# Optimization experiments

Hardware: AMD Instinct MI355X
Metric: run time of the kernel (lower is better)

The kernel has to match this reference:

```python
import jax, jax.numpy as jnp
import numpy as np

B, S, E = 8, 2048, 768
N, H = 12, 64
INIT = 0.02
IGNORE = -100000.0


def setup_inputs() -> dict:
    key = jax.random.key(0)
    ks = jax.random.split(key, 5)
    return {
        "normalized_resid_pre": jax.random.normal(ks[0], (B, S, E), jnp.float32),
        "W_Q": jax.random.normal(ks[1], (N, E, H), jnp.float32) * INIT,
        "W_K": jax.random.normal(ks[2], (N, E, H), jnp.float32) * INIT,
        "W_V": jax.random.normal(ks[3], (N, E, H), jnp.float32) * INIT,
        "W_O": jax.random.normal(ks[4], (N, H, E), jnp.float32) * INIT,
        "b_Q": jnp.zeros((N, H), jnp.float32),
        "b_K": jnp.zeros((N, H), jnp.float32),
        "b_V": jnp.zeros((N, H), jnp.float32),
        "b_O": jnp.zeros((E,), jnp.float32),
    }


def reference(normalized_resid_pre, W_Q, W_K, W_V, W_O, b_Q, b_K, b_V, b_O):
    x = normalized_resid_pre
    b, s, e = x.shape
    d_head = W_Q.shape[-1]
    q = jnp.einsum('bse,neh->bsnh', x, W_Q) + b_Q  # [b, sq, n, h]
    k = jnp.einsum('bse,neh->bsnh', x, W_K) + b_K
    v = jnp.einsum('bse,neh->bsnh', x, W_V) + b_V
    scores = jnp.einsum('bqnh,bknh->bnqk', q, k) / jnp.sqrt(jnp.float32(d_head))
    mask = jnp.tril(jnp.ones((s, s), jnp.float32))  # [sq, sk]
    masked = mask * scores + (1.0 - mask) * IGNORE
    probs = jax.nn.softmax(masked, axis=-1)
    z = jnp.einsum('bnqk,bknh->bqnh', probs, v)
    # sum over heads of per-head output projection + bias
    out = jnp.einsum('bqnh,nhe->bqe', z, W_O) + b_O
    return out
```

## Files before the change

### kernel.cpp

```cpp
#include <hip/hip_runtime.h>
#include <hip/hip_bf16.h>
#include <stdint.h>


#define B_ 8
#define S_ 2048
#define E_ 768
#define NHEADS 12
#define HD 64
#define BS (B_*S_)
#define NHD (NHEADS*HD)

typedef short bf16x8 __attribute__((ext_vector_type(8)));
typedef short bf16x4 __attribute__((ext_vector_type(4)));
typedef float f32x4  __attribute__((ext_vector_type(4)));
typedef __hip_bfloat16 bf16;

__device__ __forceinline__ f32x4 mfma16(bf16x8 a, bf16x8 b, f32x4 c) {
    return __builtin_amdgcn_mfma_f32_16x16x32_bf16(a, b, c, 0, 0, 0);
}
__device__ __forceinline__ bf16x8 ld8(const bf16* p) {
    return *reinterpret_cast<const bf16x8*>(p);
}
__device__ __forceinline__ bf16x8 pack8(f32x4 a, f32x4 b) {
    union { bf16x8 v; __hip_bfloat162 h[4]; } u;
    u.h[0] = __float22bfloat162_rn(make_float2(a[0], a[1]));
    u.h[1] = __float22bfloat162_rn(make_float2(a[2], a[3]));
    u.h[2] = __float22bfloat162_rn(make_float2(b[0], b[1]));
    u.h[3] = __float22bfloat162_rn(make_float2(b[2], b[3]));
    return u.v;
}


__global__ __launch_bounds__(256) void prep_kernel(
    const float* __restrict__ x,  const float* __restrict__ Wq,
    const float* __restrict__ Wk, const float* __restrict__ Wv,
    const float* __restrict__ Wo,
    bf16* __restrict__ xp,  bf16* __restrict__ WTp, bf16* __restrict__ WoTp)
{
    const int tid = blockIdx.x * 256 + threadIdx.x;
    const int nth = gridDim.x * 256;

    for (int c = tid; c < BS*E_/8; c += nth) {
        const int r  = c / 96;
        const int k8 = (c - r*96) * 8;
        const float4 f0 = *reinterpret_cast<const float4*>(x + (size_t)r*E_ + k8);
        const float4 f1 = *reinterpret_cast<const float4*>(x + (size_t)r*E_ + k8 + 4);
        union { bf16x8 v; __hip_bfloat162 h[4]; } u;
        u.h[0] = __float22bfloat162_rn(make_float2(f0.x, f0.y));
        u.h[1] = __float22bfloat162_rn(make_float2(f0.z, f0.w));
        u.h[2] = __float22bfloat162_rn(make_float2(f1.x, f1.y));
        u.h[3] = __float22bfloat162_rn(make_float2(f1.z, f1.w));
        const size_t dst = (size_t)((r>>4)*24 + (k8>>5))*512
                         + (size_t)((((k8>>3)&3)<<4) + (r&15))*8;
        *reinterpret_cast<bf16x8*>(xp + dst) = u.v;
    }

    for (int c2 = tid; c2 < NHD*96; c2 += nth) {
        const int r  = c2 / 96;
        const int e8 = (c2 - r*96) * 8;
        const int n = r >> 6, h = r & 63;
        const float* sq = Wq + (size_t)(n*E_ + e8)*HD + h;
        const float* sk = Wk + (size_t)(n*E_ + e8)*HD + h;
        const float* sv = Wv + (size_t)(n*E_ + e8)*HD + h;
        union { bf16x8 v; bf16 el[8]; } uq, uk, uv;
        #pragma unroll
        for (int j = 0; j < 8; ++j) {
            uq.el[j] = __float2bfloat16(sq[(size_t)j*HD]);
            uk.el[j] = __float2bfloat16(sk[(size_t)j*HD]);
            uv.el[j] = __float2bfloat16(sv[(size_t)j*HD]);
        }
        const size_t sub = (size_t)(e8>>5)*512
                         + (size_t)((((e8>>3)&3)<<4) + (r&15))*8;
        const size_t rg  = (size_t)(r>>4);
        *reinterpret_cast<bf16x8*>(WTp + ((0*48 + rg)*24)*512 + sub) = uq.v;
        *reinterpret_cast<bf16x8*>(WTp + ((1*48 + rg)*24)*512 + sub) = uk.v;
        *reinterpret_cast<bf16x8*>(WTp + ((2*48 + rg)*24)*512 + sub) = uv.v;
    }

    for (int c3 = tid; c3 < E_*96; c3 += nth) {
        const int e  = c3 / 96;
        const int c8 = (c3 - e*96) * 8;
        union { bf16x8 v; bf16 el[8]; } u;
        #pragma unroll
        for (int j = 0; j < 8; ++j)
            u.el[j] = __float2bfloat16(Wo[(size_t)(c8 + j)*E_ + e]);
        const size_t dst = (size_t)((e>>4)*24 + (c8>>5))*512
                         + (size_t)((((c8>>3)&3)<<4) + (e&15))*8;
        *reinterpret_cast<bf16x8*>(WoTp + dst) = u.v;
    }
}


#define LOAD_A(dst, base, kt, NM)                                                 \
    _Pragma("unroll") for (int m = 0; m < NM; ++m)                                \
    _Pragma("unroll") for (int ks = 0; ks < 2; ++ks)                              \
        dst[m][ks] = ld8((base) + ((size_t)m*24 + (kt)*2 + ks)*512);

#define MFMA_BLK(af, bfv, NM, NN)                                                 \
    _Pragma("unroll") for (int ks = 0; ks < 2; ++ks)                              \
    _Pragma("unroll") for (int m = 0; m < NM; ++m)                                \
    _Pragma("unroll") for (int n = 0; n < NN; ++n)                                \
        acc[m][n] = mfma16(af[m][ks], bfv[n][ks], acc[m][n]);

#define DIRECT_PIPE_BODY(Abase, Bbase, NM, NN)                                    \
    f32x4 acc[NM][NN];                                                            \
    _Pragma("unroll") for (int mf = 0; mf < NM; ++mf)                             \
    _Pragma("unroll") for (int nf = 0; nf < NN; ++nf)                             \
        acc[mf][nf] = (f32x4){0.f, 0.f, 0.f, 0.f};                                \
    bf16x8 a0[NM][2], b0[NN][2], a1[NM][2], b1[NN][2];                            \
    LOAD_A(a0, Abase, 0, NM); LOAD_A(b0, Bbase, 0, NN);                           \
    _Pragma("unroll 1")                                                           \
    for (int kk = 0; kk < 6; ++kk) {                                              \
        const int ktA = 2*kk + 1;                                                 \
        const int ktB = (2*kk + 2 < 12) ? 2*kk + 2 : 11;                          \
        LOAD_A(a1, Abase, ktA, NM); LOAD_A(b1, Bbase, ktA, NN);                   \
        __builtin_amdgcn_sched_barrier(0);                                        \
        MFMA_BLK(a0, b0, NM, NN);                                                 \
        LOAD_A(a0, Abase, ktB, NM); LOAD_A(b0, Bbase, ktB, NN);                   \
        __builtin_amdgcn_sched_barrier(0);                                        \
        MFMA_BLK(a1, b1, NM, NN);                                                 \
    }

__global__ __launch_bounds__(256, 2) void qkv_gemm_p(
    const bf16* __restrict__ xp, const bf16* __restrict__ WTp,
    const float* __restrict__ bq, const float* __restrict__ bk, const float* __restrict__ bv,
    bf16* __restrict__ Qb, bf16* __restrict__ Kb, bf16* __restrict__ VTb)
{
    const int tm = blockIdx.x, tn = blockIdx.y;
    const int lane = threadIdx.x & 63;
    const int w    = threadIdx.x >> 6;
    const int wm = w >> 1, wn = w & 1;
    const int l16 = lane & 15, quad = lane >> 4;
    const bf16* Abase = xp  + ((size_t)(tm*8 + wm*4)*24)*512 + lane*8;
    const bf16* Bbase = WTp + ((size_t)(tn*8 + wn*4)*24)*512 + lane*8;

    DIRECT_PIPE_BODY(Abase, Bbase, 4, 4);

    const int mat = tn / 6;
    const int cloc0 = (tn - mat*6)*128 + wn*64;
    const float* bias = (mat==0) ? bq : (mat==1) ? bk : bv;
    const float scale = (mat==0) ? 0.125f * 1.44269504088896340736f : 1.0f;
    bf16* dstQK = (mat==0) ? Qb : Kb;
    #pragma unroll
    for (int nf = 0; nf < 4; ++nf) {
        const int col = cloc0 + nf*16 + l16;
        const int hn = col >> 6, h = col & 63;
        const float bb = bias[col];
        #pragma unroll
        for (int mf = 0; mf < 4; ++mf) {
            const int row = tm*128 + wm*64 + mf*16 + quad*4;
            const int bi = row >> 11;
            const int s  = row & (S_-1);
            if (mat < 2) {
                bf16* d = dstQK + ((size_t)(bi*NHEADS + hn)*S_ + s)*HD + h;
                #pragma unroll
                for (int r = 0; r < 4; ++r)
                    d[(size_t)r*HD] = __float2bfloat16((acc[mf][nf][r] + bb)*scale);
            } else {
                bf16* d = VTb + ((size_t)(bi*NHEADS + hn)*HD + h)*S_ + s;
                union { bf16x4 v; bf16 e[4]; } u;
                #pragma unroll
                for (int r = 0; r < 4; ++r) u.e[r] = __float2bfloat16(acc[mf][nf][r] + bb);
                *reinterpret_cast<bf16x4*>(d) = u.v;
            }
        }
    }
}

__global__ __launch_bounds__(256, 2) void out_gemm_p(
    const bf16* __restrict__ Zp, const bf16* __restrict__ WoTp,
    const float* __restrict__ bo, float* __restrict__ out)
{
    const int tm = blockIdx.x, tn = blockIdx.y;
    const int lane = threadIdx.x & 63;
    const int w    = threadIdx.x >> 6;
    const int wm = w >> 1, wn = w & 1;
    const int l16 = lane & 15, quad = lane >> 4;
    const bf16* Abase = Zp   + ((size_t)(tm*8 + wm*4)*24)*512 + lane*8;
    const bf16* Bbase = WoTp + ((size_t)(tn*6 + wn*3)*24)*512 + lane*8;

    DIRECT_PIPE_BODY(Abase, Bbase, 4, 3);

    #pragma unroll
    for (int nf = 0; nf < 3; ++nf) {
        const int col = tn*96 + wn*48 + nf*16 + l16;
        const float bb = bo[col];
        #pragma unroll
        for (int mf = 0; mf < 4; ++mf) {
            const int row = tm*128 + wm*64 + mf*16 + quad*4;
            float* d = out + (size_t)row*E_ + col;
            #pragma unroll
            for (int r = 0; r < 4; ++r)
                d[(size_t)r*E_] = acc[mf][nf][r] + bb;
        }
    }
}

__global__ __launch_bounds__(256, 3) void attn_kernel(
    const bf16* __restrict__ Qb, const bf16* __restrict__ Kb,
    const bf16* __restrict__ VTb, bf16* __restrict__ Zp)
{
    __shared__ __align__(16) bf16 sK[2][64*64];
    __shared__ __align__(16) bf16 sV[2][64*64];

    const int id = blockIdx.x;
    const int bx = id / 96;
    const int g  = id - bx*96;
    const int hn = g % NHEADS, b = g / NHEADS;
    const int tid  = threadIdx.x;
    const int w    = tid >> 6;
    const int lane = tid & 63;
    const int l16 = lane & 15, quad = lane >> 4;
    const size_t bn = (size_t)b*NHEADS + hn;

    const bf16* Qbase = Qb  + bn*S_*HD;
    const bf16* Kbase = Kb  + bn*S_*HD;
    const bf16* Vbase = VTb + bn*HD*S_;

    const int mA = tid, mB = tid + 256;
    const int rA = mA >> 3, cgA = mA & 7;
    const int rB = mB >> 3, cgB = mB & 7;
    const int slA = (rA*8 + ((cgA + rA + (rA>>3)) & 7)) * 8;
    const int slB = (rB*8 + ((cgB + rB + (rB>>3)) & 7)) * 8;
    const size_t vofA = (size_t)rA*S_ + cgA*8;
    const size_t vofB = (size_t)rB*S_ + cgB*8;

    const int kperm = (l16 >> 2)*8 + (l16 & 3);
    int kidx[2][2][2];
    #pragma unroll
    for (int c=0;c<2;c++)
        #pragma unroll
        for (int bg=0;bg<2;bg++)
            #pragma unroll
            for (int hf=0;hf<2;hf++) {
                const int r = 32*c + 4*bg + kperm;
                const int q = hf*4 + quad;
                kidx[c][bg][hf] = (r*8 + ((q + r + (r>>3)) & 7)) * 8;
            }
    int vidx[4][2];
    #pragma unroll
    for (int ht=0;ht<4;ht++)
        #pragma unroll
        for (int c=0;c<2;c++) {
            const int rho = ht*16 + l16;
            const int q = c*4 + quad;
            vidx[ht][c] = (rho*8 + ((q + rho + (rho>>3)) & 7)) * 8;
        }

    #pragma unroll
    for (int half = 0; half < 2; ++half) {
        const int qblk = half ? (S_/128 - 1 - bx) : bx;
        const int ktb  = 2*qblk + 1;
        const int ktw  = 2*qblk + (w >> 1);
        const int qbase = qblk*128 + w*32;

        bf16x8 bqf[2][2];
        #pragma unroll
        for (int qi=0;qi<2;qi++)
            #pragma unroll
            for (int hf=0;hf<2;hf++)
                bqf[qi][hf] = ld8(Qbase + (size_t)(qbase + qi*16 + l16)*HD + hf*32 + quad*8);

        f32x4 acc[2][4];
        #pragma unroll
        for (int qi=0;qi<2;qi++)
            #pragma unroll
            for (int ht=0;ht<4;ht++) acc[qi][ht] = (f32x4){0.f,0.f,0.f,0.f};
        float lsum[2] = {0.f, 0.f};

        bf16x8 k0 = ld8(Kbase + (size_t)mA*8);
        bf16x8 k1 = ld8(Kbase + (size_t)mB*8);
        bf16x8 v0 = ld8(Vbase + vofA);
        bf16x8 v1 = ld8(Vbase + vofB);
        *reinterpret_cast<bf16x8*>(&sK[0][slA]) = k0;
        *reinterpret_cast<bf16x8*>(&sK[0][slB]) = k1;
        *reinterpret_cast<bf16x8*>(&sV[0][slA]) = v0;
        *reinterpret_cast<bf16x8*>(&sV[0][slB]) = v1;
        __syncthreads();

        for (int kt = 0; kt <= ktb; ++kt) {
            if (kt < ktb) {
                const size_t kt1 = (size_t)(kt+1)*64;
                k0 = ld8(Kbase + kt1*HD + (size_t)mA*8);
                k1 = ld8(Kbase + kt1*HD + (size_t)mB*8);
                v0 = ld8(Vbase + vofA + kt1);
                v1 = ld8(Vbase + vofB + kt1);
            }
            if (kt <= ktw) {
                const bf16* kb = sK[kt & 1];
                const bf16* vb = sV[kt & 1];
                #pragma unroll
                for (int c=0;c<2;c++) {
                    const bf16x8 akA0 = ld8(kb + kidx[c][0][0]);
                    const bf16x8 akA1 = ld8(kb + kidx[c][0][1]);
                    const bf16x8 akB0 = ld8(kb + kidx[c][1][0]);
                    const bf16x8 akB1 = ld8(kb + kidx[c][1][1]);
                    bf16x8 av[4];
                    #pragma unroll
                    for (int ht=0;ht<4;ht++) av[ht] = ld8(vb + vidx[ht][c]);

                    #pragma unroll
                    for (int qi=0;qi<2;qi++) {
                        f32x4 s0 = (f32x4){0.f,0.f,0.f,0.f};
                        s0 = mfma16(akA0, bqf[qi][0], s0);
                        s0 = mfma16(akA1, bqf[qi][1], s0);
                        f32x4 s1 = (f32x4){0.f,0.f,0.f,0.f};
                        s1 = mfma16(akB0, bqf[qi][0], s1);
                        s1 = mfma16(akB1, bqf[qi][1], s1);
                        if (kt == ktw) {
                            const int q  = qbase + qi*16 + l16;
                            const int kb0 = kt*64 + c*32 + quad*8;
                            #pragma unroll
                            for (int r=0;r<4;r++) {
                                s0[r] = (kb0 + r     > q) ? -1e30f : s0[r];
                                s1[r] = (kb0 + 4 + r > q) ? -1e30f : s1[r];
                            }
                        }
                        float ls = 0.f;
                        #pragma unroll
                        for (int r=0;r<4;r++) {
                            s0[r] = __builtin_amdgcn_exp2f(s0[r]);
                            s1[r] = __builtin_amdgcn_exp2f(s1[r]);
                            ls += s0[r] + s1[r];
                        }
                        lsum[qi] += ls;
                        const bf16x8 pf = pack8(s0, s1);
                        #pragma unroll
                        for (int ht=0;ht<4;ht++)
                            acc[qi][ht] = mfma16(av[ht], pf, acc[qi][ht]);
                    }
                }
            }
            if (kt < ktb) {
                const int nb = (kt+1) & 1;
                *reinterpret_cast<bf16x8*>(&sK[nb][slA]) = k0;
                *reinterpret_cast<bf16x8*>(&sK[nb][slB]) = k1;
                *reinterpret_cast<bf16x8*>(&sV[nb][slA]) = v0;
                *reinterpret_cast<bf16x8*>(&sV[nb][slB]) = v1;
            }
            __syncthreads();
        }

        #pragma unroll
        for (int qi=0;qi<2;qi++) {
            float rs = lsum[qi];
            rs += __shfl_xor(rs, 16, 64);
            rs += __shfl_xor(rs, 32, 64);
            const float inv_l = 1.0f / rs;
            const int rowg = b*128 + (qbase >> 4) + qi;
            #pragma unroll
            for (int ht=0;ht<4;ht++) {
                union { bf16x4 v; bf16 e[4]; } u;
                #pragma unroll
                for (int r=0;r<4;r++) u.e[r] = __float2bfloat16(acc[qi][ht][r] * inv_l);
                const int k = hn*64 + ht*16 + quad*4;
                bf16* d = Zp + ((size_t)rowg*24 + (k>>5))*512
                             + (size_t)((((k>>3)&3)<<4) + l16)*8 + (k&7);
                *reinterpret_cast<bf16x4*>(d) = u.v;
            }
        }
    }
}

extern "C" void kernel_launch(void* const* d_in, const int* in_sizes, int n_in,
                              void* d_out, int out_size, void* d_ws, size_t ws_size,
                              hipStream_t stream)
{
    const float* x  = (const float*)d_in[0];
    const float* Wq = (const float*)d_in[1];
    const float* Wk = (const float*)d_in[2];
    const float* Wv = (const float*)d_in[3];
    const float* Wo = (const float*)d_in[4];
    const float* bq = (const float*)d_in[5];
    const float* bk = (const float*)d_in[6];
    const float* bv = (const float*)d_in[7];
    const float* bo = (const float*)d_in[8];
    float* out = (float*)d_out;

    char* ws = (char*)d_ws;
    size_t off = 0;
    auto alloc = [&](size_t bytes){ char* p = ws + off; off += (bytes + 255) & ~(size_t)255; return p; };
    bf16* xp   = (bf16*)alloc((size_t)BS*E_*2);
    bf16* WTp  = (bf16*)alloc((size_t)3*NHD*E_*2);
    bf16* WoTp = (bf16*)alloc((size_t)E_*NHD*2);
    bf16* Qb   = (bf16*)alloc((size_t)BS*NHD*2);
    bf16* Kb   = (bf16*)alloc((size_t)BS*NHD*2);
    bf16* VTb  = (bf16*)alloc((size_t)BS*NHD*2);
    bf16* Zp   = (bf16*)alloc((size_t)BS*NHD*2);

    prep_kernel<<<4096, 256, 0, stream>>>(x, Wq, Wk, Wv, Wo, xp, WTp, WoTp);
    qkv_gemm_p<<<dim3(BS/128, 18), 256, 0, stream>>>(xp, WTp, bq, bk, bv, Qb, Kb, VTb);
    attn_kernel<<<768, 256, 0, stream>>>(Qb, Kb, VTb, Zp);
    out_gemm_p<<<dim3(BS/128, 8), 256, 0, stream>>>(Zp, WoTp, bo, out);
}
```

Baseline: 234.2 us.

## Triple-buffer K/V shared tiles with two-ahead prefetch and MFMA priority hints

Moves the attention kernel's K/V staging from a double buffer to a three-slot rotating LDS ring. Global loads are issued two tiles ahead, and the LDS store of the next tile happens at the top of each iteration rather than after compute. It also raises wave priority around the MFMA groups with s_setprio so matrix work from one wave is favoured over other waves' memory or ALU work. The goal is to hide more global-load latency. In exchange LDS use grows from 32KB to 48KB per block, which may reduce occupancy under launch_bounds(256,3). The initial prefetch of tile 1 also reads past the end of the tile range when ktb is 0.

```diff
diff --git a/kernel.cpp b/kernel.cpp
--- a/kernel.cpp
+++ b/kernel.cpp
@@ -201,8 +201,8 @@
     const bf16* __restrict__ Qb, const bf16* __restrict__ Kb,
     const bf16* __restrict__ VTb, bf16* __restrict__ Zp)
 {
-    __shared__ __align__(16) bf16 sK[2][64*64];
-    __shared__ __align__(16) bf16 sV[2][64*64];
+    __shared__ __align__(16) bf16 sK[3*4096];
+    __shared__ __align__(16) bf16 sV[3*4096];
 
     const int id = blockIdx.x;
     const int bx = id / 96;
@@ -273,23 +273,36 @@
         bf16x8 k1 = ld8(Kbase + (size_t)mB*8);
         bf16x8 v0 = ld8(Vbase + vofA);
         bf16x8 v1 = ld8(Vbase + vofB);
-        *reinterpret_cast<bf16x8*>(&sK[0][slA]) = k0;
-        *reinterpret_cast<bf16x8*>(&sK[0][slB]) = k1;
-        *reinterpret_cast<bf16x8*>(&sV[0][slA]) = v0;
-        *reinterpret_cast<bf16x8*>(&sV[0][slB]) = v1;
+        *reinterpret_cast<bf16x8*>(&sK[slA]) = k0;
+        *reinterpret_cast<bf16x8*>(&sK[slB]) = k1;
+        *reinterpret_cast<bf16x8*>(&sV[slA]) = v0;
+        *reinterpret_cast<bf16x8*>(&sV[slB]) = v1;
+        k0 = ld8(Kbase + 4096 + (size_t)mA*8);
+        k1 = ld8(Kbase + 4096 + (size_t)mB*8);
+        v0 = ld8(Vbase + vofA + 64);
+        v1 = ld8(Vbase + vofB + 64);
         __syncthreads();
 
+        int rd = 0, wr = 1, l3 = 2;
         for (int kt = 0; kt <= ktb; ++kt) {
-            if (kt < ktb) {
-                const size_t kt1 = (size_t)(kt+1)*64;
-                k0 = ld8(Kbase + kt1*HD + (size_t)mA*8);
-                k1 = ld8(Kbase + kt1*HD + (size_t)mB*8);
-                v0 = ld8(Vbase + vofA + kt1);
-                v1 = ld8(Vbase + vofB + kt1);
+            if (kt + 1 <= ktb) {
+                bf16* kw = sK + wr*4096;
+                bf16* vw = sV + wr*4096;
+                *reinterpret_cast<bf16x8*>(&kw[slA]) = k0;
+                *reinterpret_cast<bf16x8*>(&kw[slB]) = k1;
+                *reinterpret_cast<bf16x8*>(&vw[slA]) = v0;
+                *reinterpret_cast<bf16x8*>(&vw[slB]) = v1;
+            }
+            if (kt + 2 <= ktb) {
+                const size_t o = (size_t)(kt + 2) * 64;
+                k0 = ld8(Kbase + o*HD + (size_t)mA*8);
+                k1 = ld8(Kbase + o*HD + (size_t)mB*8);
+                v0 = ld8(Vbase + vofA + o);
+                v1 = ld8(Vbase + vofB + o);
             }
             if (kt <= ktw) {
-                const bf16* kb = sK[kt & 1];
-                const bf16* vb = sV[kt & 1];
+                const bf16* kb = sK + rd*4096;
+                const bf16* vb = sV + rd*4096;
                 #pragma unroll
                 for (int c=0;c<2;c++) {
                     const bf16x8 akA0 = ld8(kb + kidx[c][0][0]);
@@ -302,12 +315,14 @@
 
                     #pragma unroll
                     for (int qi=0;qi<2;qi++) {
+                        __builtin_amdgcn_s_setprio(1);
                         f32x4 s0 = (f32x4){0.f,0.f,0.f,0.f};
                         s0 = mfma16(akA0, bqf[qi][0], s0);
                         s0 = mfma16(akA1, bqf[qi][1], s0);
                         f32x4 s1 = (f32x4){0.f,0.f,0.f,0.f};
                         s1 = mfma16(akB0, bqf[qi][0], s1);
                         s1 = mfma16(akB1, bqf[qi][1], s1);
+                        __builtin_amdgcn_s_setprio(0);
                         if (kt == ktw) {
                             const int q  = qbase + qi*16 + l16;
                             const int kb0 = kt*64 + c*32 + quad*8;
@@ -326,20 +341,16 @@
                         }
                         lsum[qi] += ls;
                         const bf16x8 pf = pack8(s0, s1);
+                        __builtin_amdgcn_s_setprio(1);
                         #pragma unroll
                         for (int ht=0;ht<4;ht++)
                             acc[qi][ht] = mfma16(av[ht], pf, acc[qi][ht]);
+                        __builtin_amdgcn_s_setprio(0);
                     }
                 }
             }
-            if (kt < ktb) {
-                const int nb = (kt+1) & 1;
-                *reinterpret_cast<bf16x8*>(&sK[nb][slA]) = k0;
-                *reinterpret_cast<bf16x8*>(&sK[nb][slB]) = k1;
-                *reinterpret_cast<bf16x8*>(&sV[nb][slA]) = v0;
-                *reinterpret_cast<bf16x8*>(&sV[nb][slB]) = v1;
-            }
             __syncthreads();
+            const int t = rd; rd = wr; wr = l3; l3 = t;
         }
 
         #pragma unroll
```

After: 232.8 us. Within noise of the previous version (-0.6%).

## Pre-swizzle K/V into MFMA fragment layout and drop LDS staging in attention

Applied to the files above, without the earlier changes.

The QKV GEMM epilogue now writes K and V directly in a packed per-fragment layout, so each lane can load MFMA operands from global memory with one 16-byte load. The attention kernel drops the shared-memory double buffer and __syncthreads, and each wave now handles 64 query rows independently with a register-level software pipeline over 32-key chunks. This removes LDS traffic and block-wide barriers, at the cost of more register pressure (occupancy hint lowered to 2) and scattered 2-byte stores for K in the GEMM epilogue. Each wave now reads K/V from global or L2 on its own instead of sharing one staged copy per block.

```diff
diff --git a/kernel.cpp b/kernel.cpp
--- a/kernel.cpp
+++ b/kernel.cpp
@@ -125,7 +125,7 @@
 __global__ __launch_bounds__(256, 2) void qkv_gemm_p(
     const bf16* __restrict__ xp, const bf16* __restrict__ WTp,
     const float* __restrict__ bq, const float* __restrict__ bk, const float* __restrict__ bv,
-    bf16* __restrict__ Qb, bf16* __restrict__ Kb, bf16* __restrict__ VTb)
+    bf16* __restrict__ Qb, bf16* __restrict__ Kp, bf16* __restrict__ Vp)
 {
     const int tm = blockIdx.x, tn = blockIdx.y;
     const int lane = threadIdx.x & 63;
@@ -141,7 +141,6 @@
     const int cloc0 = (tn - mat*6)*128 + wn*64;
     const float* bias = (mat==0) ? bq : (mat==1) ? bk : bv;
     const float scale = (mat==0) ? 0.125f * 1.44269504088896340736f : 1.0f;
-    bf16* dstQK = (mat==0) ? Qb : Kb;
     #pragma unroll
     for (int nf = 0; nf < 4; ++nf) {
         const int col = cloc0 + nf*16 + l16;
@@ -152,16 +151,33 @@
             const int row = tm*128 + wm*64 + mf*16 + quad*4;
             const int bi = row >> 11;
             const int s  = row & (S_-1);
-            if (mat < 2) {
-                bf16* d = dstQK + ((size_t)(bi*NHEADS + hn)*S_ + s)*HD + h;
+            const size_t headbase = (size_t)(bi*NHEADS + hn)*256*512;
+            if (mat == 0) {
+                bf16* d = Qb + ((size_t)(bi*NHEADS + hn)*S_ + s)*HD + h;
                 #pragma unroll
                 for (int r = 0; r < 4; ++r)
                     d[(size_t)r*HD] = __float2bfloat16((acc[mf][nf][r] + bb)*scale);
+            } else if (mat == 1) {
+                const int hf = h >> 5, kq = (h >> 3) & 3, e = h & 7;
+                #pragma unroll
+                for (int r = 0; r < 4; ++r) {
+                    const int sr = s + r;
+                    const int gg = sr >> 5, kv5 = sr & 31;
+                    const int bg = (kv5 >> 2) & 1;
+                    const int rl = ((kv5 >> 3) << 2) | (kv5 & 3);
+                    Kp[headbase + (size_t)(gg*4 + bg*2 + hf)*512 + (kq*16 + rl)*8 + e]
+                        = __float2bfloat16(acc[mf][nf][r] + bb);
+                }
             } else {
-                bf16* d = VTb + ((size_t)(bi*NHEADS + hn)*HD + h)*S_ + s;
+                const int dg = (h >> 4) & 3;
+                const int rl = h & 15;
+                const int gg = s >> 5;
+                const int kq = (s >> 3) & 3;
+                const int e0 = s & 7;
                 union { bf16x4 v; bf16 e[4]; } u;
                 #pragma unroll
                 for (int r = 0; r < 4; ++r) u.e[r] = __float2bfloat16(acc[mf][nf][r] + bb);
+                bf16* d = Vp + headbase + (size_t)(gg*4 + dg)*512 + (kq*16 + rl)*8 + e0;
                 *reinterpret_cast<bf16x4*>(d) = u.v;
             }
         }
@@ -197,170 +213,113 @@
     }
 }
 
-__global__ __launch_bounds__(256, 3) void attn_kernel(
-    const bf16* __restrict__ Qb, const bf16* __restrict__ Kb,
-    const bf16* __restrict__ VTb, bf16* __restrict__ Zp)
-{
-    __shared__ __align__(16) bf16 sK[2][64*64];
-    __shared__ __align__(16) bf16 sV[2][64*64];
-
+__global__ __launch_bounds__(256, 2) void attn_kernel(
+    const bf16* __restrict__ Qb, const bf16* __restrict__ Kp,
+    const bf16* __restrict__ Vp, bf16* __restrict__ Zp)
+{
     const int id = blockIdx.x;
     const int bx = id / 96;
-    const int g  = id - bx*96;
-    const int hn = g % NHEADS, b = g / NHEADS;
-    const int tid  = threadIdx.x;
-    const int w    = tid >> 6;
-    const int lane = tid & 63;
+    const int hc = id - bx*96;
+    const int hn = hc % NHEADS, b = hc / NHEADS;
+    const int w    = threadIdx.x >> 6;
+    const int lane = threadIdx.x & 63;
     const int l16 = lane & 15, quad = lane >> 4;
     const size_t bn = (size_t)b*NHEADS + hn;
 
-    const bf16* Qbase = Qb  + bn*S_*HD;
-    const bf16* Kbase = Kb  + bn*S_*HD;
-    const bf16* Vbase = VTb + bn*HD*S_;
-
-    const int mA = tid, mB = tid + 256;
-    const int rA = mA >> 3, cgA = mA & 7;
-    const int rB = mB >> 3, cgB = mB & 7;
-    const int slA = (rA*8 + ((cgA + rA + (rA>>3)) & 7)) * 8;
-    const int slB = (rB*8 + ((cgB + rB + (rB>>3)) & 7)) * 8;
-    const size_t vofA = (size_t)rA*S_ + cgA*8;
-    const size_t vofB = (size_t)rB*S_ + cgB*8;
-
-    const int kperm = (l16 >> 2)*8 + (l16 & 3);
-    int kidx[2][2][2];
-    #pragma unroll
-    for (int c=0;c<2;c++)
-        #pragma unroll
-        for (int bg=0;bg<2;bg++)
+    const int qblk = (w >> 1) ? (15 - bx) : bx;
+    const int wsub = w & 1;
+    const int qbase = qblk*128 + wsub*64;
+    const int jmax  = 2*(2*qblk + wsub) + 1;
+
+    const bf16* Qbase = Qb + bn*(size_t)S_*HD;
+    const bf16* Kh = Kp + bn*(size_t)256*512;
+    const bf16* Vh = Vp + bn*(size_t)256*512;
+
+    bf16x8 bqf[4][2];
+    #pragma unroll
+    for (int qi = 0; qi < 4; ++qi)
+        #pragma unroll
+        for (int hf = 0; hf < 2; ++hf)
+            bqf[qi][hf] = ld8(Qbase + (size_t)(qbase + qi*16 + l16)*HD + hf*32 + quad*8);
+
+    f32x4 acc[4][4];
+    #pragma unroll
+    for (int qi = 0; qi < 4; ++qi)
+        #pragma unroll
+        for (int ht = 0; ht < 4; ++ht) acc[qi][ht] = (f32x4){0.f,0.f,0.f,0.f};
+    float lsum[4] = {0.f, 0.f, 0.f, 0.f};
+
+#define LD_KV(ks, vs, gj) do {                                                    \
+    _Pragma("unroll") for (int f = 0; f < 4; ++f)                                 \
+        ks[f] = ld8(Kh + ((size_t)(gj)*4 + f)*512 + lane*8);                      \
+    _Pragma("unroll") for (int f = 0; f < 4; ++f)                                 \
+        vs[f] = ld8(Vh + ((size_t)(gj)*4 + f)*512 + lane*8);                      \
+} while (0)
+
+#define ATT_COMPUTE(ks, vs, j) do {                                               \
+    const int kvbase = (j) * 32;                                                  \
+    const bool diag = (kvbase + 31 > qbase);                                      \
+    _Pragma("unroll")                                                             \
+    for (int qi = 0; qi < 4; ++qi) {                                              \
+        f32x4 s0 = (f32x4){0.f,0.f,0.f,0.f};                                      \
+        s0 = mfma16(ks[0], bqf[qi][0], s0);                                       \
+        s0 = mfma16(ks[1], bqf[qi][1], s0);                                       \
+        f32x4 s1 = (f32x4){0.f,0.f,0.f,0.f};                                      \
+        s1 = mfma16(ks[2], bqf[qi][0], s1);                                       \
+        s1 = mfma16(ks[3], bqf[qi][1], s1);                                       \
+        if (diag) {                                                               \
+            const int q   = qbase + qi*16 + l16;                                  \
+            const int kb0 = kvbase + quad*8;                                      \
+            _Pragma("unroll") for (int r = 0; r < 4; ++r) {                       \
+                s0[r] = (kb0 + r     > q) ? -1e30f : s0[r];                       \
+                s1[r] = (kb0 + 4 + r > q) ? -1e30f : s1[r];                       \
+            }                                                                     \
+        }                                                                         \
+        float ls = 0.f;                                                           \
+        _Pragma("unroll") for (int r = 0; r < 4; ++r) {                           \
+            s0[r] = __builtin_amdgcn_exp2f(s0[r]);                                \
+            s1[r] = __builtin_amdgcn_exp2f(s1[r]);                                \
+            ls += s0[r] + s1[r];                                                  \
+        }                                                                         \
+        lsum[qi] += ls;                                                           \
+        const bf16x8 pf = pack8(s0, s1);                                          \
+        _Pragma("unroll") for (int ht = 0; ht < 4; ++ht)                          \
+            acc[qi][ht] = mfma16(vs[ht], pf, acc[qi][ht]);                        \
+    }                                                                             \
+} while (0)
+
+    bf16x8 k0[4], v0[4], k1[4], v1[4];
+    LD_KV(k0, v0, 0);
+    #pragma unroll 1
+    for (int j = 0; j < jmax; j += 2) {
+        LD_KV(k1, v1, j + 1);
+        __builtin_amdgcn_sched_barrier(0);
+        ATT_COMPUTE(k0, v0, j);
+        if (j + 2 <= jmax) { LD_KV(k0, v0, j + 2); }
+        __builtin_amdgcn_sched_barrier(0);
+        ATT_COMPUTE(k1, v1, j + 1);
+    }
+
+    #pragma unroll
+    for (int qi = 0; qi < 4; ++qi) {
+        float rs = lsum[qi];
+        rs += __shfl_xor(rs, 16, 64);
+        rs += __shfl_xor(rs, 32, 64);
+        const float inv_l = 1.0f / rs;
+        const int rowg = b*128 + (qbase >> 4) + qi;
+        #pragma unroll
+        for (int ht = 0; ht < 4; ++ht) {
+            union { bf16x4 v; bf16 e[4]; } u;
             #pragma unroll
-            for (int hf=0;hf<2;hf++) {
-                const int r = 32*c + 4*bg + kperm;
-                const int q = hf*4 + quad;
-                kidx[c][bg][hf] = (r*8 + ((q + r + (r>>3)) & 7)) * 8;
-            }
-    int vidx[4][2];
-    #pragma unroll
-    for (int ht=0;ht<4;ht++)
-        #pragma unroll
-        for (int c=0;c<2;c++) {
-            const int rho = ht*16 + l16;
-            const int q = c*4 + quad;
-            vidx[ht][c] = (rho*8 + ((q + rho + (rho>>3)) & 7)) * 8;
+            for (int r = 0; r < 4; ++r) u.e[r] = __float2bfloat16(acc[qi][ht][r] * inv_l);
+            const int k = hn*64 + ht*16 + quad*4;
+            bf16* d = Zp + ((size_t)rowg*24 + (k>>5))*512
+                         + (size_t)((((k>>3)&3)<<4) + l16)*8 + (k&7);
+            *reinterpret_cast<bf16x4*>(d) = u.v;
         }
-
-    #pragma unroll
-    for (int half = 0; half < 2; ++half) {
-        const int qblk = half ? (S_/128 - 1 - bx) : bx;
-        const int ktb  = 2*qblk + 1;
-        const int ktw  = 2*qblk + (w >> 1);
-        const int qbase = qblk*128 + w*32;
-
-        bf16x8 bqf[2][2];
-        #pragma unroll
-        for (int qi=0;qi<2;qi++)
-            #pragma unroll
-            for (int hf=0;hf<2;hf++)
-                bqf[qi][hf] = ld8(Qbase + (size_t)(qbase + qi*16 + l16)*HD + hf*32 + quad*8);
-
-        f32x4 acc[2][4];
-        #pragma unroll
-        for (int qi=0;qi<2;qi++)
-            #pragma unroll
-            for (int ht=0;ht<4;ht++) acc[qi][ht] = (f32x4){0.f,0.f,0.f,0.f};
-        float lsum[2] = {0.f, 0.f};
-
-        bf16x8 k0 = ld8(Kbase + (size_t)mA*8);
-        bf16x8 k1 = ld8(Kbase + (size_t)mB*8);
-        bf16x8 v0 = ld8(Vbase + vofA);
-        bf16x8 v1 = ld8(Vbase + vofB);
-        *reinterpret_cast<bf16x8*>(&sK[0][slA]) = k0;
-        *reinterpret_cast<bf16x8*>(&sK[0][slB]) = k1;
-        *reinterpret_cast<bf16x8*>(&sV[0][slA]) = v0;
-        *reinterpret_cast<bf16x8*>(&sV[0][slB]) = v1;
-        __syncthreads();
-
-        for (int kt = 0; kt <= ktb; ++kt) {
-            if (kt < ktb) {
-                const size_t kt1 = (size_t)(kt+1)*64;
-                k0 = ld8(Kbase + kt1*HD + (size_t)mA*8);
-                k1 = ld8(Kbase + kt1*HD + (size_t)mB*8);
-                v0 = ld8(Vbase + vofA + kt1);
-                v1 = ld8(Vbase + vofB + kt1);
-            }
-            if (kt <= ktw) {
-                const bf16* kb = sK[kt & 1];
-                const bf16* vb = sV[kt & 1];
-                #pragma unroll
-                for (int c=0;c<2;c++) {
-                    const bf16x8 akA0 = ld8(kb + kidx[c][0][0]);
-                    const bf16x8 akA1 = ld8(kb + kidx[c][0][1]);
-                    const bf16x8 akB0 = ld8(kb + kidx[c][1][0]);
-                    const bf16x8 akB1 = ld8(kb + kidx[c][1][1]);
-                    bf16x8 av[4];
-                    #pragma unroll
-                    for (int ht=0;ht<4;ht++) av[ht] = ld8(vb + vidx[ht][c]);
-
-                    #pragma unroll
-                    for (int qi=0;qi<2;qi++) {
-                        f32x4 s0 = (f32x4){0.f,0.f,0.f,0.f};
-                        s0 = mfma16(akA0, bqf[qi][0], s0);
-                        s0 = mfma16(akA1, bqf[qi][1], s0);
-                        f32x4 s1 = (f32x4){0.f,0.f,0.f,0.f};
-                        s1 = mfma16(akB0, bqf[qi][0], s1);
-                        s1 = mfma16(akB1, bqf[qi][1], s1);
-                        if (kt == ktw) {
-                            const int q  = qbase + qi*16 + l16;
-                            const int kb0 = kt*64 + c*32 + quad*8;
-                            #pragma unroll
-                            for (int r=0;r<4;r++) {
-                                s0[r] = (kb0 + r     > q) ? -1e30f : s0[r];
-                                s1[r] = (kb0 + 4 + r > q) ? -1e30f : s1[r];
-                            }
-                        }
-                        float ls = 0.f;
-                        #pragma unroll
-                        for (int r=0;r<4;r++) {
-                            s0[r] = __builtin_amdgcn_exp2f(s0[r]);
-                            s1[r] = __builtin_amdgcn_exp2f(s1[r]);
-                            ls += s0[r] + s1[r];
-                        }
-                        lsum[qi] += ls;
-                        const bf16x8 pf = pack8(s0, s1);
-                        #pragma unroll
-                        for (int ht=0;ht<4;ht++)
-                            acc[qi][ht] = mfma16(av[ht], pf, acc[qi][ht]);
-                    }
-                }
-            }
-            if (kt < ktb) {
-                const int nb = (kt+1) & 1;
-                *reinterpret_cast<bf16x8*>(&sK[nb][slA]) = k0;
-                *reinterpret_cast<bf16x8*>(&sK[nb][slB]) = k1;
-                *reinterpret_cast<bf16x8*>(&sV[nb][slA]) = v0;
-                *reinterpret_cast<bf16x8*>(&sV[nb][slB]) = v1;
-            }
-            __syncthreads();
-        }
-
-        #pragma unroll
-        for (int qi=0;qi<2;qi++) {
-            float rs = lsum[qi];
-            rs += __shfl_xor(rs, 16, 64);
-            rs += __shfl_xor(rs, 32, 64);
-            const float inv_l = 1.0f / rs;
-            const int rowg = b*128 + (qbase >> 4) + qi;
-            #pragma unroll
-            for (int ht=0;ht<4;ht++) {
-                union { bf16x4 v; bf16 e[4]; } u;
-                #pragma unroll
-                for (int r=0;r<4;r++) u.e[r] = __float2bfloat16(acc[qi][ht][r] * inv_l);
-                const int k = hn*64 + ht*16 + quad*4;
-                bf16* d = Zp + ((size_t)rowg*24 + (k>>5))*512
-                             + (size_t)((((k>>3)&3)<<4) + l16)*8 + (k&7);
-                *reinterpret_cast<bf16x4*>(d) = u.v;
-            }
-        }
-    }
+    }
+#undef LD_KV
+#undef ATT_COMPUTE
 }
 
 extern "C" void kernel_launch(void* const* d_in, const int* in_sizes, int n_in,
@@ -385,12 +344,12 @@
     bf16* WTp  = (bf16*)alloc((size_t)3*NHD*E_*2);
     bf16* WoTp = (bf16*)alloc((size_t)E_*NHD*2);
     bf16* Qb   = (bf16*)alloc((size_t)BS*NHD*2);
-    bf16* Kb   = (bf16*)alloc((size_t)BS*NHD*2);
-    bf16* VTb  = (bf16*)alloc((size_t)BS*NHD*2);
+    bf16* Kp   = (bf16*)alloc((size_t)BS*NHD*2);
+    bf16* Vp   = (bf16*)alloc((size_t)BS*NHD*2);
     bf16* Zp   = (bf16*)alloc((size_t)BS*NHD*2);
 
     prep_kernel<<<4096, 256, 0, stream>>>(x, Wq, Wk, Wv, Wo, xp, WTp, WoTp);
-    qkv_gemm_p<<<dim3(BS/128, 18), 256, 0, stream>>>(xp, WTp, bq, bk, bv, Qb, Kb, VTb);
-    attn_kernel<<<768, 256, 0, stream>>>(Qb, Kb, VTb, Zp);
+    qkv_gemm_p<<<dim3(BS/128, 18), 256, 0, stream>>>(xp, WTp, bq, bk, bv, Qb, Kp, Vp);
+    attn_kernel<<<768, 256, 0, stream>>>(Qb, Kp, Vp, Zp);
     out_gemm_p<<<dim3(BS/128, 8), 256, 0, stream>>>(Zp, WoTp, bo, out);
 }
```

New measurement: 240.7 us. +2.8%, slower.
